# Optimization experiments

Measured on AMD Instinct MI355X. Metric: run time of the kernel, lower is better.

## Reference

```python
import jax, jax.numpy as jnp
import numpy as np

INPUT_SIZE = 1024
HIDDEN_SIZE = 1024
W_RANK = 64
U_RANK = 64
BATCH = 32768


def setup_inputs() -> dict:
    key = jax.random.key(0)
    ks = jax.random.split(key, 16)
    p = lambda k, shape: 0.1 * jax.random.normal(k, shape, dtype=jnp.float32)
    return {
        "x": jax.random.normal(ks[0], (BATCH, INPUT_SIZE), dtype=jnp.float32),
        "h": jax.random.normal(ks[1], (BATCH, HIDDEN_SIZE), dtype=jnp.float32),
        "W": p(ks[2], (INPUT_SIZE, W_RANK)),
        "W1": p(ks[3], (W_RANK, HIDDEN_SIZE)),
        "W2": p(ks[4], (W_RANK, HIDDEN_SIZE)),
        "W3": p(ks[5], (W_RANK, HIDDEN_SIZE)),
        "U": p(ks[6], (HIDDEN_SIZE, U_RANK)),
        "U1": p(ks[7], (U_RANK, HIDDEN_SIZE)),
        "U2": p(ks[8], (U_RANK, HIDDEN_SIZE)),
        "U3": p(ks[9], (U_RANK, HIDDEN_SIZE)),
        "U1_diag": p(ks[10], (HIDDEN_SIZE,)),
        "U2_diag": p(ks[11], (HIDDEN_SIZE,)),
        "U3_diag": p(ks[12], (HIDDEN_SIZE,)),
        "bias_r": jnp.ones((1, HIDDEN_SIZE), dtype=jnp.float32),
        "bias_gate": jnp.ones((1, HIDDEN_SIZE), dtype=jnp.float32),
        "bias_update": jnp.ones((1, HIDDEN_SIZE), dtype=jnp.float32),
    }


def reference(x, h, W, W1, W2, W3, U, U1, U2, U3,
              U1_diag, U2_diag, U3_diag, bias_r, bias_gate, bias_update):
    # Low-rank projections shared across gates (matches torch matmul order)
    xW = x @ W          # [B, wRank]
    hU = h @ U          # [B, uRank]
    wVal1 = xW @ W1
    wVal2 = xW @ W2
    wVal3 = xW @ W3
    uVal1 = hU @ U1
    uVal2 = hU @ U2
    r = jax.nn.sigmoid(wVal1 + uVal1 + h * U1_diag + bias_r)
    z = jax.nn.sigmoid(wVal2 + uVal2 + h * U2_diag + bias_gate)
    rh = r * h
    matVal_c = wVal3 + (rh @ U) @ U3 + rh * U3_diag
    c_tilda = jnp.tanh(matVal_c + bias_update)
    h_next = z * h + (1.0 - z) * c_tilda
    return h_next
```

## Files before the change

### kernel.cpp

```cpp
#include <hip/hip_runtime.h>
#include <hip/hip_bf16.h>


typedef __attribute__((ext_vector_type(8))) short short8;
typedef __attribute__((ext_vector_type(4))) float f32x4;
typedef __attribute__((ext_vector_type(4))) float f4;

#define WS_UT   65536
#define WS_P1T  131072
#define WS_P2T  262144
#define WS_P3T  393216
#define WS_A12  524288
#define WS_RHU  4718592

__device__ __forceinline__ short f2bf(float f) {
  unsigned u = __builtin_bit_cast(unsigned, f);
  u += 0x7FFFu + ((u >> 16) & 1u);
  return (short)(u >> 16);
}
__device__ __forceinline__ short8 cvt8(f4 a, f4 b) {
  short8 r;
#pragma unroll
  for (int j = 0; j < 4; ++j) { r[j] = f2bf(a[j]); r[4 + j] = f2bf(b[j]); }
  return r;
}
__device__ __forceinline__ f32x4 mfma16(short8 a, short8 b, f32x4 c) {
  return __builtin_amdgcn_mfma_f32_16x16x32_bf16(a, b, c, 0, 0, 0);
}
__device__ __forceinline__ short8 ldg8(const short* p) {
  return *reinterpret_cast<const short8*>(p);
}

__device__ __forceinline__ void cp16(void* l, const void* g) {
  __builtin_amdgcn_global_load_lds(
      (const __attribute__((address_space(1))) void*)g,
      (__attribute__((address_space(3))) void*)l, 16, 0, 0);
}
#define VWAIT(N) do { asm volatile("s_waitcnt vmcnt(" #N ")" ::: "memory"); \
                      __builtin_amdgcn_sched_barrier(0); } while (0)

__device__ __forceinline__ short8 rd128s(const short* b, int row, int col) {
  return *reinterpret_cast<const short8*>(b + row * 128 + (col ^ ((row & 7) << 3)));
}
__device__ __forceinline__ void wr128s(short* b, int row, int col8, short8 v) {
  *reinterpret_cast<short8*>(b + row * 128 + (col8 ^ ((row & 7) << 3))) = v;
}
__device__ __forceinline__ void wr64(short* b, int row, int col, short v) {
  b[row * 64 + (col ^ ((row & 7) << 3))] = v;
}
__device__ __forceinline__ short8 rd64(const short* b, int row, int col) {
  return *reinterpret_cast<const short8*>(b + row * 64 + (col ^ ((row & 7) << 3)));
}

#define LOG2E 1.4426950408889634f
__device__ __forceinline__ float sigm_f(float v) {
  return __builtin_amdgcn_rcpf(1.f + __builtin_amdgcn_exp2f(-v * LOG2E));
}
__device__ __forceinline__ float tanh_f(float v) {
  float t = __builtin_amdgcn_exp2f(v * (2.f * LOG2E));
  return 1.f - 2.f * __builtin_amdgcn_rcpf(t + 1.f);
}

__global__ void prep_kernel(const float* __restrict__ W,  const float* __restrict__ W1,
                            const float* __restrict__ W2, const float* __restrict__ W3,
                            const float* __restrict__ U,  const float* __restrict__ U1,
                            const float* __restrict__ U2, const float* __restrict__ U3,
                            short* __restrict__ ws) {
  int i = blockIdx.x * blockDim.x + threadIdx.x;
  float v;
  if (i < 65536) {
    int n = i >> 10, k = i & 1023;
    v = W[k * 64 + n];
  } else if (i < 131072) {
    int j = i - 65536;
    int n = j >> 10, k = j & 1023;
    v = U[k * 64 + n];
  } else {
    int j = i - 131072;
    int sel = j >> 17;
    int jj = j & 131071;
    int n = jj >> 7, k = jj & 127;
    const float* Wk = sel == 0 ? W1 : sel == 1 ? W2 : W3;
    const float* Uk = sel == 0 ? U1 : sel == 1 ? U2 : U3;
    v = (k < 64) ? Wk[k * 1024 + n] : Uk[(k - 64) * 1024 + n];
  }
  ws[i] = f2bf(v);
}

__global__ __launch_bounds__(256, 2) void k1_a12(
    const float* __restrict__ x, const float* __restrict__ h,
    const short* __restrict__ ws, short* __restrict__ A12) {
  __shared__ __align__(16) float sS[2][4][16 * 128];

  const int tid = threadIdx.x;
  const int w = tid >> 6, l = tid & 63, l15 = l & 15, lg = l >> 4;
  const int m = w >> 1, half = w & 1;
  const int sr = blockIdx.x * 32 + half * 16;
  const float* src = m ? h : x;
  const short* Bt  = ws + m * WS_UT;

  const int srow = l >> 5;
  const int slin = (l & 31) * 16;

  auto STAGE = [&](int c, int b) {
#pragma unroll
    for (int i = 0; i < 8; ++i) {
      int r = i * 2 + srow;
      int kb = slin ^ ((r & 7) << 4);
      cp16((char*)&sS[b][w][0] + i * 1024,
           (const char*)(src + (size_t)(sr + r) * 1024 + c * 128) + kb);
    }
  };

  f32x4 acc[4] = {};
  STAGE(0, 0);
#pragma unroll 1
  for (int c = 0; c < 8; ++c) {
    short8 bw[4][4];
#pragma unroll
    for (int ks = 0; ks < 4; ++ks)
#pragma unroll
      for (int cf = 0; cf < 4; ++cf)
        bw[ks][cf] = ldg8(Bt + (size_t)(cf * 16 + l15) * 1024 + c * 128 + ks * 32 + lg * 8);
    if (c < 7) { STAGE(c + 1, (c + 1) & 1); VWAIT(8); }
    else       { VWAIT(0); }
    const char* Bb = (const char*)&sS[c & 1][w][0];
    const int s = (l15 & 7) << 4;
#pragma unroll
    for (int ks = 0; ks < 4; ++ks) {
      const int kb0 = (ks * 32 + lg * 8) * 4;
      f4 pa = *(const f4*)(Bb + l15 * 512 + (kb0 ^ s));
      f4 pb = *(const f4*)(Bb + l15 * 512 + ((kb0 + 16) ^ s));
      short8 av = cvt8(pa, pb);
#pragma unroll
      for (int cf = 0; cf < 4; ++cf) acc[cf] = mfma16(av, bw[ks][cf], acc[cf]);
    }
  }
#pragma unroll
  for (int cf = 0; cf < 4; ++cf)
#pragma unroll
    for (int j = 0; j < 4; ++j)
      A12[(size_t)(sr + lg * 4 + j) * 128 + m * 64 + cf * 16 + l15] = f2bf(acc[cf][j]);
}

__global__ __launch_bounds__(256, 2) void k23_rhu(
    const float* __restrict__ h, const float* __restrict__ u1d,
    const float* __restrict__ biasR,
    const short* __restrict__ ws, const short* __restrict__ A12,
    short* __restrict__ rhU) {
  const short* Ut  = ws + WS_UT;
  const short* P1t = ws + WS_P1T;
  __shared__ __align__(16) float hS[2][4][16 * 64];
  __shared__ __align__(16) short sT[4][16 * 64];

  const int tid = threadIdx.x;
  const int w = tid >> 6, l = tid & 63, l15 = l & 15, lg = l >> 4;
  const int sr = blockIdx.x * 64 + w * 16;

  const int srow = l >> 4;
  const int slin = (l & 15) * 16;

  auto STAGE = [&](int t, int b) {
#pragma unroll
    for (int i = 0; i < 4; ++i) {
      int r = i * 4 + srow;
      int kb = slin ^ ((r & 7) << 4);
      cp16((char*)&hS[b][w][0] + i * 1024,
           (const char*)(h + (size_t)(sr + r) * 1024 + t * 64) + kb);
    }
  };

  short8 a12[4];
#pragma unroll
  for (int k0 = 0; k0 < 4; ++k0)
    a12[k0] = ldg8(A12 + (size_t)(sr + l15) * 128 + k0 * 32 + lg * 8);

  f32x4 accU[4] = {};
  STAGE(0, 0);
#pragma unroll 1
  for (int tt = 0; tt < 16; ++tt) {
    const int n0 = tt * 64;
    short8 b1[4][4], bu[2][4];
    float d1_[4], br_[4];
#pragma unroll
    for (int ks = 0; ks < 4; ++ks)
#pragma unroll
      for (int cf = 0; cf < 4; ++cf)
        b1[ks][cf] = ldg8(P1t + (size_t)(n0 + cf * 16 + l15) * 128 + ks * 32 + lg * 8);
#pragma unroll
    for (int kk = 0; kk < 2; ++kk)
#pragma unroll
      for (int cf = 0; cf < 4; ++cf)
        bu[kk][cf] = ldg8(Ut + (size_t)(cf * 16 + l15) * 1024 + n0 + kk * 32 + lg * 8);
#pragma unroll
    for (int cf = 0; cf < 4; ++cf) {
      d1_[cf] = u1d[n0 + cf * 16 + l15];
      br_[cf] = biasR[n0 + cf * 16 + l15];
    }
    if (tt < 15) { STAGE(tt + 1, (tt + 1) & 1); VWAIT(4); }
    else         { VWAIT(0); }
    const char* H = (const char*)&hS[tt & 1][w][0];

    float hv[4][4];
#pragma unroll
    for (int cf = 0; cf < 4; ++cf)
#pragma unroll
      for (int j = 0; j < 4; ++j) {
        int rr = lg * 4 + j;
        hv[cf][j] = *(const float*)(H + rr * 256 + ((cf * 64 + l15 * 4) ^ ((rr & 7) << 4)));
      }
    f32x4 accR[4] = {};
#pragma unroll
    for (int ks = 0; ks < 4; ++ks)
#pragma unroll
      for (int cf = 0; cf < 4; ++cf) accR[cf] = mfma16(a12[ks], b1[ks][cf], accR[cf]);
#pragma unroll
    for (int cf = 0; cf < 4; ++cf)
#pragma unroll
      for (int j = 0; j < 4; ++j) {
        float rv = sigm_f(accR[cf][j] + hv[cf][j] * d1_[cf] + br_[cf]);
        wr64(&sT[w][0], lg * 4 + j, cf * 16 + l15, f2bf(rv * hv[cf][j]));
      }
    short8 arh0 = rd64(&sT[w][0], l15, lg * 8);
    short8 arh1 = rd64(&sT[w][0], l15, 32 + lg * 8);
#pragma unroll
    for (int cf = 0; cf < 4; ++cf) accU[cf] = mfma16(arh0, bu[0][cf], accU[cf]);
#pragma unroll
    for (int cf = 0; cf < 4; ++cf) accU[cf] = mfma16(arh1, bu[1][cf], accU[cf]);
  }
#pragma unroll
  for (int cf = 0; cf < 4; ++cf)
#pragma unroll
    for (int j = 0; j < 4; ++j)
      rhU[(size_t)(sr + lg * 4 + j) * 64 + cf * 16 + l15] = f2bf(accU[cf][j]);
}

__global__ __launch_bounds__(256, 2) void k4_out(
    const float* __restrict__ h,
    const float* __restrict__ u1d, const float* __restrict__ u2d,
    const float* __restrict__ u3d,
    const float* __restrict__ biasR, const float* __restrict__ biasZ,
    const float* __restrict__ biasU,
    const short* __restrict__ ws, const short* __restrict__ A12,
    const short* __restrict__ rhU, float* __restrict__ out) {
  __shared__ __align__(16) short sB1[64 * 128], sB2[64 * 128], sB3[64 * 128];
  __shared__ __align__(16) float hS[2][4][16 * 64];

  const int tid = threadIdx.x;
  const int w = tid >> 6, l = tid & 63, l15 = l & 15, lg = l >> 4;
  const int ct = blockIdx.x & 15, rc = blockIdx.x >> 4;
  const int n0 = ct * 64;

#pragma unroll
  for (int mat = 0; mat < 3; ++mat) {
    const short* srcw = (mat == 0) ? (ws + WS_P1T) : (mat == 1) ? (ws + WS_P2T) : (ws + WS_P3T);
    short* dst = (mat == 0) ? sB1 : (mat == 1) ? sB2 : sB3;
#pragma unroll
    for (int i = 0; i < 4; ++i) {
      int id = tid + i * 256;
      int row = id >> 4, gc = id & 15;
      wr128s(dst, row, gc * 8, ldg8(srcw + (size_t)(n0 + row) * 128 + gc * 8));
    }
  }
  float d1_[4], d2_[4], d3_[4], br_[4], bz_[4], bu_[4];
#pragma unroll
  for (int cf = 0; cf < 4; ++cf) {
    const int cc = n0 + cf * 16 + l15;
    d1_[cf] = u1d[cc]; d2_[cf] = u2d[cc]; d3_[cf] = u3d[cc];
    br_[cf] = biasR[cc]; bz_[cf] = biasZ[cc]; bu_[cf] = biasU[cc];
  }
  __syncthreads();

  const int srow = l >> 4;
  const int slin = (l & 15) * 16;
  auto STAGE = [&](int rnd, int b) {
    const int sb = rc * 512 + rnd * 64 + w * 16;
#pragma unroll
    for (int i = 0; i < 4; ++i) {
      int r = i * 4 + srow;
      int kb = slin ^ ((r & 7) << 4);
      cp16((char*)&hS[b][w][0] + i * 1024,
           (const char*)(h + (size_t)(sb + r) * 1024 + n0) + kb);
    }
  };

  STAGE(0, 0);
#pragma unroll 1
  for (int rnd = 0; rnd < 8; ++rnd) {
    const int sr = rc * 512 + rnd * 64 + w * 16;
    short8 a12[4], arhu[2];
#pragma unroll
    for (int k0 = 0; k0 < 4; ++k0)
      a12[k0] = ldg8(A12 + (size_t)(sr + l15) * 128 + k0 * 32 + lg * 8);
#pragma unroll
    for (int kk = 0; kk < 2; ++kk)
      arhu[kk] = ldg8(rhU + (size_t)(sr + l15) * 64 + kk * 32 + lg * 8);
    if (rnd < 7) { STAGE(rnd + 1, (rnd + 1) & 1); VWAIT(4); }
    else         { VWAIT(0); }
    const char* H = (const char*)&hS[rnd & 1][w][0];

    float hv[4][4];
#pragma unroll
    for (int cf = 0; cf < 4; ++cf)
#pragma unroll
      for (int j = 0; j < 4; ++j) {
        int rr = lg * 4 + j;
        hv[cf][j] = *(const float*)(H + rr * 256 + ((cf * 64 + l15 * 4) ^ ((rr & 7) << 4)));
      }

    f32x4 aR[4] = {}, aZ[4] = {}, aC[4] = {};
#pragma unroll
    for (int k0 = 0; k0 < 4; ++k0) {
      const short8 a3 = (k0 < 2) ? a12[k0] : arhu[k0 - 2];
#pragma unroll
      for (int cf = 0; cf < 4; ++cf) {
        aR[cf] = mfma16(a12[k0], rd128s(sB1, cf * 16 + l15, k0 * 32 + lg * 8), aR[cf]);
        aZ[cf] = mfma16(a12[k0], rd128s(sB2, cf * 16 + l15, k0 * 32 + lg * 8), aZ[cf]);
        aC[cf] = mfma16(a3,      rd128s(sB3, cf * 16 + l15, k0 * 32 + lg * 8), aC[cf]);
      }
    }
#pragma unroll
    for (int cf = 0; cf < 4; ++cf) {
      const int cc = n0 + cf * 16 + l15;
#pragma unroll
      for (int j = 0; j < 4; ++j) {
        const size_t gi = (size_t)(sr + lg * 4 + j) * 1024 + cc;
        const float hvj = hv[cf][j];
        float rv = sigm_f(aR[cf][j] + hvj * d1_[cf] + br_[cf]);
        float zv = sigm_f(aZ[cf][j] + hvj * d2_[cf] + bz_[cf]);
        float cv = tanh_f(aC[cf][j] + rv * hvj * d3_[cf] + bu_[cf]);
        out[gi] = zv * hvj + (1.f - zv) * cv;
      }
    }
  }
}

extern "C" void kernel_launch(void* const* d_in, const int* in_sizes, int n_in,
                              void* d_out, int out_size, void* d_ws, size_t ws_size,
                              hipStream_t stream) {
  const float* x   = (const float*)d_in[0];
  const float* h   = (const float*)d_in[1];
  const float* W   = (const float*)d_in[2];
  const float* W1  = (const float*)d_in[3];
  const float* W2  = (const float*)d_in[4];
  const float* W3  = (const float*)d_in[5];
  const float* U   = (const float*)d_in[6];
  const float* U1  = (const float*)d_in[7];
  const float* U2  = (const float*)d_in[8];
  const float* U3  = (const float*)d_in[9];
  const float* u1d = (const float*)d_in[10];
  const float* u2d = (const float*)d_in[11];
  const float* u3d = (const float*)d_in[12];
  const float* bR  = (const float*)d_in[13];
  const float* bZ  = (const float*)d_in[14];
  const float* bU  = (const float*)d_in[15];
  short* ws  = (short*)d_ws;
  short* A12 = ws + WS_A12;
  short* rhU = ws + WS_RHU;

  prep_kernel<<<2048, 256, 0, stream>>>(W, W1, W2, W3, U, U1, U2, U3, ws);
  k1_a12<<<1024, 256, 0, stream>>>(x, h, ws, A12);
  k23_rhu<<<512, 256, 0, stream>>>(h, u1d, bR, ws, A12, rhU);
  k4_out<<<1024, 256, 0, stream>>>(h, u1d, u2d, u3d, bR, bZ, bU, ws, A12, rhU, (float*)d_out);
}
```

Before: 251.9 us.

## Restructure k1 to tile 64 rows per block with bf16 LDS staging

The first projection kernel now gives each block 64 rows of both x and h. Each wave computes both the x·W and h·U products for its 16 rows, sharing B-fragment loads across a larger tile. The fp32 inputs are loaded with plain vector loads, converted to bf16 once and written to swizzled LDS, replacing async global-to-LDS copies of fp32 and per-wave conversion. This halves LDS use and raises occupancy to 4 blocks per CU. The trade-off is losing the double-buffered async prefetch: loads are now synchronous with two barriers per chunk, and B fragments are fetched inside the MFMA loop instead of being prefetched.

```diff
diff --git a/kernel.cpp b/kernel.cpp
--- a/kernel.cpp
+++ b/kernel.cpp
@@ -5,6 +5,7 @@
 typedef __attribute__((ext_vector_type(8))) short short8;
 typedef __attribute__((ext_vector_type(4))) float f32x4;
 typedef __attribute__((ext_vector_type(4))) float f4;
+typedef __attribute__((ext_vector_type(2))) unsigned int uint2v;
 
 #define WS_UT   65536
 #define WS_P1T  131072
@@ -18,6 +19,9 @@
   u += 0x7FFFu + ((u >> 16) & 1u);
   return (short)(u >> 16);
 }
+__device__ __forceinline__ unsigned pack2(float a, float b) {
+  return (unsigned)(unsigned short)f2bf(a) | ((unsigned)(unsigned short)f2bf(b) << 16);
+}
 __device__ __forceinline__ short8 cvt8(f4 a, f4 b) {
   short8 r;
 #pragma unroll
@@ -29,6 +33,9 @@
 }
 __device__ __forceinline__ short8 ldg8(const short* p) {
   return *reinterpret_cast<const short8*>(p);
+}
+__device__ __forceinline__ f4 ldf4(const float* p) {
+  return *reinterpret_cast<const f4*>(p);
 }
 
 __device__ __forceinline__ void cp16(void* l, const void* g) {
@@ -87,60 +94,72 @@
   ws[i] = f2bf(v);
 }
 
-__global__ __launch_bounds__(256, 2) void k1_a12(
+__global__ __launch_bounds__(256, 4) void k1_a12(
     const float* __restrict__ x, const float* __restrict__ h,
     const short* __restrict__ ws, short* __restrict__ A12) {
-  __shared__ __align__(16) float sS[2][4][16 * 128];
+  __shared__ __align__(16) short sX[64 * 128];
+  __shared__ __align__(16) short sH[64 * 128];
 
   const int tid = threadIdx.x;
   const int w = tid >> 6, l = tid & 63, l15 = l & 15, lg = l >> 4;
-  const int m = w >> 1, half = w & 1;
-  const int sr = blockIdx.x * 32 + half * 16;
-  const float* src = m ? h : x;
-  const short* Bt  = ws + m * WS_UT;
-
-  const int srow = l >> 5;
-  const int slin = (l & 31) * 16;
-
-  auto STAGE = [&](int c, int b) {
-#pragma unroll
-    for (int i = 0; i < 8; ++i) {
-      int r = i * 2 + srow;
-      int kb = slin ^ ((r & 7) << 4);
-      cp16((char*)&sS[b][w][0] + i * 1024,
-           (const char*)(src + (size_t)(sr + r) * 1024 + c * 128) + kb);
-    }
-  };
-
-  f32x4 acc[4] = {};
-  STAGE(0, 0);
+  const int r0 = blockIdx.x * 64;
+  const short* Wt = ws;
+  const short* Ut = ws + WS_UT;
+
+  const int strow = tid >> 5;
+  const int sc4   = tid & 31;
+
+  f32x4 accX[4] = {}, accH[4] = {};
+
 #pragma unroll 1
   for (int c = 0; c < 8; ++c) {
-    short8 bw[4][4];
-#pragma unroll
-    for (int ks = 0; ks < 4; ++ks)
-#pragma unroll
-      for (int cf = 0; cf < 4; ++cf)
-        bw[ks][cf] = ldg8(Bt + (size_t)(cf * 16 + l15) * 1024 + c * 128 + ks * 32 + lg * 8);
-    if (c < 7) { STAGE(c + 1, (c + 1) & 1); VWAIT(8); }
-    else       { VWAIT(0); }
-    const char* Bb = (const char*)&sS[c & 1][w][0];
-    const int s = (l15 & 7) << 4;
+    {
+      f4 xv[8], hv[8];
+#pragma unroll
+      for (int i = 0; i < 8; ++i) {
+        const int row = i * 8 + strow;
+        xv[i] = ldf4(x + (size_t)(r0 + row) * 1024 + c * 128 + sc4 * 4);
+        hv[i] = ldf4(h + (size_t)(r0 + row) * 1024 + c * 128 + sc4 * 4);
+      }
+#pragma unroll
+      for (int i = 0; i < 8; ++i) {
+        const int row = i * 8 + strow;
+        const int off = row * 128 + ((sc4 * 4) ^ ((row & 7) << 3));
+        uint2v px, ph;
+        px.x = pack2(xv[i][0], xv[i][1]); px.y = pack2(xv[i][2], xv[i][3]);
+        ph.x = pack2(hv[i][0], hv[i][1]); ph.y = pack2(hv[i][2], hv[i][3]);
+        *reinterpret_cast<uint2v*>(&sX[off]) = px;
+        *reinterpret_cast<uint2v*>(&sH[off]) = ph;
+      }
+    }
+    __syncthreads();
+
 #pragma unroll
     for (int ks = 0; ks < 4; ++ks) {
-      const int kb0 = (ks * 32 + lg * 8) * 4;
-      f4 pa = *(const f4*)(Bb + l15 * 512 + (kb0 ^ s));
-      f4 pb = *(const f4*)(Bb + l15 * 512 + ((kb0 + 16) ^ s));
-      short8 av = cvt8(pa, pb);
-#pragma unroll
-      for (int cf = 0; cf < 4; ++cf) acc[cf] = mfma16(av, bw[ks][cf], acc[cf]);
-    }
-  }
+      short8 ax = rd128s(sX, 16 * w + l15, ks * 32 + lg * 8);
+      short8 ah = rd128s(sH, 16 * w + l15, ks * 32 + lg * 8);
+#pragma unroll
+      for (int cf = 0; cf < 4; ++cf) {
+        short8 bw = ldg8(Wt + (size_t)(cf * 16 + l15) * 1024 + c * 128 + ks * 32 + lg * 8);
+        accX[cf] = mfma16(ax, bw, accX[cf]);
+      }
+#pragma unroll
+      for (int cf = 0; cf < 4; ++cf) {
+        short8 bu = ldg8(Ut + (size_t)(cf * 16 + l15) * 1024 + c * 128 + ks * 32 + lg * 8);
+        accH[cf] = mfma16(ah, bu, accH[cf]);
+      }
+    }
+    __syncthreads();
+  }
+
 #pragma unroll
   for (int cf = 0; cf < 4; ++cf)
 #pragma unroll
-    for (int j = 0; j < 4; ++j)
-      A12[(size_t)(sr + lg * 4 + j) * 128 + m * 64 + cf * 16 + l15] = f2bf(acc[cf][j]);
+    for (int j = 0; j < 4; ++j) {
+      const size_t rr = (size_t)(r0 + 16 * w + lg * 4 + j) * 128;
+      A12[rr + cf * 16 + l15]      = f2bf(accX[cf][j]);
+      A12[rr + 64 + cf * 16 + l15] = f2bf(accH[cf][j]);
+    }
 }
 
 __global__ __launch_bounds__(256, 2) void k23_rhu(
@@ -359,7 +378,7 @@
   short* rhU = ws + WS_RHU;
 
   prep_kernel<<<2048, 256, 0, stream>>>(W, W1, W2, W3, U, U1, U2, U3, ws);
-  k1_a12<<<1024, 256, 0, stream>>>(x, h, ws, A12);
+  k1_a12<<<512, 256, 0, stream>>>(x, h, ws, A12);
   k23_rhu<<<512, 256, 0, stream>>>(h, u1d, bR, ws, A12, rhU);
   k4_out<<<1024, 256, 0, stream>>>(h, u1d, u2d, u3d, bR, bZ, bU, ws, A12, rhU, (float*)d_out);
 }
```

Measured after the change: 295.5 us. +17.3%, slower.

## Restructure output kernel to one tile per wave and halve k1 staging

Applied to the files above, without the earlier changes.

The output kernel drops its LDS staging of the three projection matrices and of h. Each wave now handles a single 16-row by 64-column tile, reading weights straight from global memory and h directly, and the grid grows to 8192 blocks with a swizzled block-to-tile mapping. The first projection kernel halves its LDS staging chunk to 64 columns over 16 iterations, and both kernels raise the occupancy hint to 4 blocks per CU. This aims to cut LDS usage and the per-block weight-load preamble so more waves can hide latency. The cost is more global and L2 traffic for the weights and uncoalesced per-element h loads.

```diff
diff --git a/kernel.cpp b/kernel.cpp
--- a/kernel.cpp
+++ b/kernel.cpp
@@ -30,6 +30,9 @@
 __device__ __forceinline__ short8 ldg8(const short* p) {
   return *reinterpret_cast<const short8*>(p);
 }
+__device__ __forceinline__ f4 ldf4(const float* p) {
+  return *reinterpret_cast<const f4*>(p);
+}
 
 __device__ __forceinline__ void cp16(void* l, const void* g) {
   __builtin_amdgcn_global_load_lds(
@@ -39,12 +42,6 @@
 #define VWAIT(N) do { asm volatile("s_waitcnt vmcnt(" #N ")" ::: "memory"); \
                       __builtin_amdgcn_sched_barrier(0); } while (0)
 
-__device__ __forceinline__ short8 rd128s(const short* b, int row, int col) {
-  return *reinterpret_cast<const short8*>(b + row * 128 + (col ^ ((row & 7) << 3)));
-}
-__device__ __forceinline__ void wr128s(short* b, int row, int col8, short8 v) {
-  *reinterpret_cast<short8*>(b + row * 128 + (col8 ^ ((row & 7) << 3))) = v;
-}
 __device__ __forceinline__ void wr64(short* b, int row, int col, short v) {
   b[row * 64 + (col ^ ((row & 7) << 3))] = v;
 }
@@ -87,10 +84,10 @@
   ws[i] = f2bf(v);
 }
 
-__global__ __launch_bounds__(256, 2) void k1_a12(
+__global__ __launch_bounds__(256, 4) void k1_a12(
     const float* __restrict__ x, const float* __restrict__ h,
     const short* __restrict__ ws, short* __restrict__ A12) {
-  __shared__ __align__(16) float sS[2][4][16 * 128];
+  __shared__ __align__(16) float sS[2][4][16 * 64];
 
   const int tid = threadIdx.x;
   const int w = tid >> 6, l = tid & 63, l15 = l & 15, lg = l >> 4;
@@ -99,38 +96,38 @@
   const float* src = m ? h : x;
   const short* Bt  = ws + m * WS_UT;
 
-  const int srow = l >> 5;
-  const int slin = (l & 31) * 16;
+  const int srow = l >> 4;
+  const int slin = (l & 15) * 16;
 
   auto STAGE = [&](int c, int b) {
 #pragma unroll
-    for (int i = 0; i < 8; ++i) {
-      int r = i * 2 + srow;
+    for (int i = 0; i < 4; ++i) {
+      int r = i * 4 + srow;
       int kb = slin ^ ((r & 7) << 4);
       cp16((char*)&sS[b][w][0] + i * 1024,
-           (const char*)(src + (size_t)(sr + r) * 1024 + c * 128) + kb);
+           (const char*)(src + (size_t)(sr + r) * 1024 + c * 64) + kb);
     }
   };
 
   f32x4 acc[4] = {};
   STAGE(0, 0);
 #pragma unroll 1
-  for (int c = 0; c < 8; ++c) {
-    short8 bw[4][4];
-#pragma unroll
-    for (int ks = 0; ks < 4; ++ks)
+  for (int c = 0; c < 16; ++c) {
+    short8 bw[2][4];
+#pragma unroll
+    for (int ks = 0; ks < 2; ++ks)
 #pragma unroll
       for (int cf = 0; cf < 4; ++cf)
-        bw[ks][cf] = ldg8(Bt + (size_t)(cf * 16 + l15) * 1024 + c * 128 + ks * 32 + lg * 8);
-    if (c < 7) { STAGE(c + 1, (c + 1) & 1); VWAIT(8); }
-    else       { VWAIT(0); }
+        bw[ks][cf] = ldg8(Bt + (size_t)(cf * 16 + l15) * 1024 + c * 64 + ks * 32 + lg * 8);
+    if (c < 15) { STAGE(c + 1, (c + 1) & 1); VWAIT(4); }
+    else        { VWAIT(0); }
     const char* Bb = (const char*)&sS[c & 1][w][0];
     const int s = (l15 & 7) << 4;
 #pragma unroll
-    for (int ks = 0; ks < 4; ++ks) {
+    for (int ks = 0; ks < 2; ++ks) {
       const int kb0 = (ks * 32 + lg * 8) * 4;
-      f4 pa = *(const f4*)(Bb + l15 * 512 + (kb0 ^ s));
-      f4 pb = *(const f4*)(Bb + l15 * 512 + ((kb0 + 16) ^ s));
+      f4 pa = *(const f4*)(Bb + l15 * 256 + (kb0 ^ s));
+      f4 pb = *(const f4*)(Bb + l15 * 256 + ((kb0 + 16) ^ s));
       short8 av = cvt8(pa, pb);
 #pragma unroll
       for (int cf = 0; cf < 4; ++cf) acc[cf] = mfma16(av, bw[ks][cf], acc[cf]);
@@ -235,7 +232,7 @@
       rhU[(size_t)(sr + lg * 4 + j) * 64 + cf * 16 + l15] = f2bf(accU[cf][j]);
 }
 
-__global__ __launch_bounds__(256, 2) void k4_out(
+__global__ __launch_bounds__(256, 4) void k4_out(
     const float* __restrict__ h,
     const float* __restrict__ u1d, const float* __restrict__ u2d,
     const float* __restrict__ u3d,
@@ -243,94 +240,52 @@
     const float* __restrict__ biasU,
     const short* __restrict__ ws, const short* __restrict__ A12,
     const short* __restrict__ rhU, float* __restrict__ out) {
-  __shared__ __align__(16) short sB1[64 * 128], sB2[64 * 128], sB3[64 * 128];
-  __shared__ __align__(16) float hS[2][4][16 * 64];
+  const short* P1t = ws + WS_P1T;
+  const short* P2t = ws + WS_P2T;
+  const short* P3t = ws + WS_P3T;
+
+  const int b = (blockIdx.x & 7) * 1024 + (blockIdx.x >> 3);
 
   const int tid = threadIdx.x;
   const int w = tid >> 6, l = tid & 63, l15 = l & 15, lg = l >> 4;
-  const int ct = blockIdx.x & 15, rc = blockIdx.x >> 4;
-  const int n0 = ct * 64;
-
-#pragma unroll
-  for (int mat = 0; mat < 3; ++mat) {
-    const short* srcw = (mat == 0) ? (ws + WS_P1T) : (mat == 1) ? (ws + WS_P2T) : (ws + WS_P3T);
-    short* dst = (mat == 0) ? sB1 : (mat == 1) ? sB2 : sB3;
-#pragma unroll
-    for (int i = 0; i < 4; ++i) {
-      int id = tid + i * 256;
-      int row = id >> 4, gc = id & 15;
-      wr128s(dst, row, gc * 8, ldg8(srcw + (size_t)(n0 + row) * 128 + gc * 8));
-    }
-  }
-  float d1_[4], d2_[4], d3_[4], br_[4], bz_[4], bu_[4];
+  const int gw = b * 4 + w;
+  const int sr = (gw >> 4) * 16;
+  const int n0 = (gw & 15) * 64;
+
+  short8 a12[4], arhu[2];
+#pragma unroll
+  for (int k0 = 0; k0 < 4; ++k0)
+    a12[k0] = ldg8(A12 + (size_t)(sr + l15) * 128 + k0 * 32 + lg * 8);
+#pragma unroll
+  for (int kk = 0; kk < 2; ++kk)
+    arhu[kk] = ldg8(rhU + (size_t)(sr + l15) * 64 + kk * 32 + lg * 8);
+
+  f32x4 aR[4] = {}, aZ[4] = {}, aC[4] = {};
+#pragma unroll
+  for (int ks = 0; ks < 4; ++ks) {
+    const short8 a3 = (ks < 2) ? a12[ks] : arhu[ks - 2];
+#pragma unroll
+    for (int cf = 0; cf < 4; ++cf) {
+      const size_t bo = (size_t)(n0 + cf * 16 + l15) * 128 + ks * 32 + lg * 8;
+      aR[cf] = mfma16(a12[ks], ldg8(P1t + bo), aR[cf]);
+      aZ[cf] = mfma16(a12[ks], ldg8(P2t + bo), aZ[cf]);
+      aC[cf] = mfma16(a3,      ldg8(P3t + bo), aC[cf]);
+    }
+  }
+
 #pragma unroll
   for (int cf = 0; cf < 4; ++cf) {
     const int cc = n0 + cf * 16 + l15;
-    d1_[cf] = u1d[cc]; d2_[cf] = u2d[cc]; d3_[cf] = u3d[cc];
-    br_[cf] = biasR[cc]; bz_[cf] = biasZ[cc]; bu_[cf] = biasU[cc];
-  }
-  __syncthreads();
-
-  const int srow = l >> 4;
-  const int slin = (l & 15) * 16;
-  auto STAGE = [&](int rnd, int b) {
-    const int sb = rc * 512 + rnd * 64 + w * 16;
-#pragma unroll
-    for (int i = 0; i < 4; ++i) {
-      int r = i * 4 + srow;
-      int kb = slin ^ ((r & 7) << 4);
-      cp16((char*)&hS[b][w][0] + i * 1024,
-           (const char*)(h + (size_t)(sb + r) * 1024 + n0) + kb);
-    }
-  };
-
-  STAGE(0, 0);
-#pragma unroll 1
-  for (int rnd = 0; rnd < 8; ++rnd) {
-    const int sr = rc * 512 + rnd * 64 + w * 16;
-    short8 a12[4], arhu[2];
-#pragma unroll
-    for (int k0 = 0; k0 < 4; ++k0)
-      a12[k0] = ldg8(A12 + (size_t)(sr + l15) * 128 + k0 * 32 + lg * 8);
-#pragma unroll
-    for (int kk = 0; kk < 2; ++kk)
-      arhu[kk] = ldg8(rhU + (size_t)(sr + l15) * 64 + kk * 32 + lg * 8);
-    if (rnd < 7) { STAGE(rnd + 1, (rnd + 1) & 1); VWAIT(4); }
-    else         { VWAIT(0); }
-    const char* H = (const char*)&hS[rnd & 1][w][0];
-
-    float hv[4][4];
-#pragma unroll
-    for (int cf = 0; cf < 4; ++cf)
-#pragma unroll
-      for (int j = 0; j < 4; ++j) {
-        int rr = lg * 4 + j;
-        hv[cf][j] = *(const float*)(H + rr * 256 + ((cf * 64 + l15 * 4) ^ ((rr & 7) << 4)));
-      }
-
-    f32x4 aR[4] = {}, aZ[4] = {}, aC[4] = {};
-#pragma unroll
-    for (int k0 = 0; k0 < 4; ++k0) {
-      const short8 a3 = (k0 < 2) ? a12[k0] : arhu[k0 - 2];
-#pragma unroll
-      for (int cf = 0; cf < 4; ++cf) {
-        aR[cf] = mfma16(a12[k0], rd128s(sB1, cf * 16 + l15, k0 * 32 + lg * 8), aR[cf]);
-        aZ[cf] = mfma16(a12[k0], rd128s(sB2, cf * 16 + l15, k0 * 32 + lg * 8), aZ[cf]);
-        aC[cf] = mfma16(a3,      rd128s(sB3, cf * 16 + l15, k0 * 32 + lg * 8), aC[cf]);
-      }
-    }
-#pragma unroll
-    for (int cf = 0; cf < 4; ++cf) {
-      const int cc = n0 + cf * 16 + l15;
-#pragma unroll
-      for (int j = 0; j < 4; ++j) {
-        const size_t gi = (size_t)(sr + lg * 4 + j) * 1024 + cc;
-        const float hvj = hv[cf][j];
-        float rv = sigm_f(aR[cf][j] + hvj * d1_[cf] + br_[cf]);
-        float zv = sigm_f(aZ[cf][j] + hvj * d2_[cf] + bz_[cf]);
-        float cv = tanh_f(aC[cf][j] + rv * hvj * d3_[cf] + bu_[cf]);
-        out[gi] = zv * hvj + (1.f - zv) * cv;
-      }
+    const float d1 = u1d[cc], d2 = u2d[cc], d3 = u3d[cc];
+    const float b_r = biasR[cc], b_z = biasZ[cc], b_u = biasU[cc];
+#pragma unroll
+    for (int j = 0; j < 4; ++j) {
+      const size_t gi = (size_t)(sr + lg * 4 + j) * 1024 + cc;
+      const float hvj = h[gi];
+      float rv = sigm_f(aR[cf][j] + hvj * d1 + b_r);
+      float zv = sigm_f(aZ[cf][j] + hvj * d2 + b_z);
+      float cv = tanh_f(aC[cf][j] + rv * hvj * d3 + b_u);
+      out[gi] = zv * hvj + (1.f - zv) * cv;
     }
   }
 }
@@ -361,5 +316,5 @@
   prep_kernel<<<2048, 256, 0, stream>>>(W, W1, W2, W3, U, U1, U2, U3, ws);
   k1_a12<<<1024, 256, 0, stream>>>(x, h, ws, A12);
   k23_rhu<<<512, 256, 0, stream>>>(h, u1d, bR, ws, A12, rhU);
-  k4_out<<<1024, 256, 0, stream>>>(h, u1d, u2d, u3d, bR, bZ, bU, ws, A12, rhU, (float*)d_out);
-}
+  k4_out<<<8192, 256, 0, stream>>>(h, u1d, u2d, u3d, bR, bZ, bU, ws, A12, rhU, (float*)d_out);
+}
```

After: 399.9 us. 1.59x slower.
